# Performance work log

Measured on AMD Instinct MI355X. Metric: run time of the kernel, lower is better.

Reference implementation:

```python
import jax, jax.numpy as jnp
import numpy as np

L, H, C, HS, E, K, V, BS = 2, 12, 768, 64, 8, 2, 32000, 1024
B, T = 2, 1024


def layer_norm(x, s, b):
    mu = x.mean(-1, keepdims=True)
    var = ((x - mu) ** 2).mean(-1, keepdims=True)
    return (x - mu) / jnp.sqrt(var + 1e-5) * s + b


def setup_inputs() -> dict:
    key = jax.random.key(0)
    ks = jax.random.split(key, 16)
    def n(k, shape, s=0.02):
        return jax.random.normal(k, shape, dtype=jnp.float32) * s
    return {
        'idx': jax.random.randint(ks[0], (B, T), 0, V),
        'targets': jax.random.randint(ks[1], (B, T), 0, V),
        'tok_emb': n(ks[2], (V, C)),
        'pos_emb': n(ks[3], (BS, C)),
        'ln1_s': jnp.ones((L, C), jnp.float32), 'ln1_b': jnp.zeros((L, C), jnp.float32),
        'wq': n(ks[4], (L, H, C, HS)), 'wk': n(ks[5], (L, H, C, HS)), 'wv': n(ks[6], (L, H, C, HS)),
        'wo': n(ks[7], (L, C, C)), 'bo': jnp.zeros((L, C), jnp.float32),
        'ln2_s': jnp.ones((L, C), jnp.float32), 'ln2_b': jnp.zeros((L, C), jnp.float32),
        'gate_w': n(ks[8], (L, E, C)),
        'w1': n(ks[9], (L, E, 4 * C, C)), 'b1': jnp.zeros((L, E, 4 * C), jnp.float32),
        'w2': n(ks[10], (L, E, C, 4 * C)), 'b2': jnp.zeros((L, E, C), jnp.float32),
        'lm_w': n(ks[11], (V, C)), 'lm_b': jnp.zeros((V,), jnp.float32),
    }


def reference(idx, targets, tok_emb, pos_emb, ln1_s, ln1_b, wq, wk, wv, wo, bo,
              ln2_s, ln2_b, gate_w, w1, b1, w2, b2, lm_w, lm_b):
    Bsz, Tn = idx.shape
    x = tok_emb[idx] + pos_emb[:Tn]                       # [B,T,C]
    mask = jnp.tril(jnp.ones((Tn, Tn), bool))
    for l in range(L):
        # causal multi-head attention (per-head projections, scale = n_embed**-0.5 as in source)
        h = layer_norm(x, ln1_s[l], ln1_b[l])
        q = jnp.einsum('btc,hcd->bhtd', h, wq[l])
        k = jnp.einsum('btc,hcd->bhtd', h, wk[l])
        v = jnp.einsum('btc,hcd->bhtd', h, wv[l])
        att = jnp.einsum('bhtd,bhsd->bhts', q, k) * (C ** -0.5)
        att = jax.nn.softmax(jnp.where(mask, att, -jnp.inf), axis=-1)
        o = jnp.einsum('bhts,bhsd->bhtd', att, v)
        o = o.transpose(0, 2, 1, 3).reshape(Bsz, Tn, C)   # concat heads
        x = x + jnp.einsum('btc,oc->bto', o, wo[l]) + bo[l]
        # MoE FFN: top-k routing, softmax over selected gate logits
        h2 = layer_norm(x, ln2_s[l], ln2_b[l]).reshape(-1, C)     # [N,C]
        gl = jnp.einsum('tc,ec->te', h2, gate_w[l])               # [N,E]
        wts, sel = jax.lax.top_k(gl, K)
        wts = jax.nn.softmax(wts, axis=-1)
        comb = jnp.einsum('tk,tke->te', wts, jax.nn.one_hot(sel, E, dtype=wts.dtype))
        hid = jax.nn.relu(jnp.einsum('tc,efc->etf', h2, w1[l]) + b1[l][:, None, :])
        y = jnp.einsum('etf,ecf->etc', hid, w2[l]) + b2[l][:, None, :]
        moe = jnp.einsum('te,etc->tc', comb, y)                   # dispatch-weighted combine
        x = x + moe.reshape(Bsz, Tn, C)
    logits = jnp.einsum('btc,vc->btv', x, lm_w) + lm_b
    lf = logits.reshape(-1, V)
    tf = targets.reshape(-1)
    loss = -jnp.take_along_axis(jax.nn.log_softmax(lf, axis=-1), tf[:, None], axis=1).mean()
    return lf, loss
```

## Files before the change

### kernel.cpp

```cpp
#include <hip/hip_runtime.h>
#include <hip/hip_bf16.h>

#define LCNT 2
#define HCNT 12
#define CDIM 768
#define HSD  64
#define ECNT 8
#define VOC  32000
#define BB   2
#define TT   1024
#define NTOK 2048
#define FF   3072
#define QKVLD 2304
#define TOTCAP 5120

typedef __attribute__((ext_vector_type(8))) short bf16x8;
typedef __attribute__((ext_vector_type(4))) float f32x4;

__device__ __forceinline__ float wave_sum(float v) {
    #pragma unroll
    for (int off = 32; off; off >>= 1) v += __shfl_xor(v, off);
    return v;
}
__device__ __forceinline__ float wave_max(float v) {
    #pragma unroll
    for (int off = 32; off; off >>= 1) v = fmaxf(v, __shfl_xor(v, off));
    return v;
}
__device__ __forceinline__ unsigned short f2bf(float f) {
    unsigned int u = __float_as_uint(f);
    unsigned int r = (u + 0x7FFFu + ((u >> 16) & 1u)) >> 16;
    return (unsigned short)r;
}
__device__ __forceinline__ float bf2f(unsigned short h) {
    return __uint_as_float((unsigned int)h << 16);
}
__device__ __forceinline__ void split2(float a, unsigned short& h, unsigned short& l) {
    h = f2bf(a);
    l = f2bf(a - bf2f(h));
}
__device__ __forceinline__ ushort4 cvt4(float4 v) {
    ushort4 r;
    r.x = f2bf(v.x); r.y = f2bf(v.y); r.z = f2bf(v.z); r.w = f2bf(v.w);
    return r;
}
__device__ __forceinline__ void gload16(const void* g, void* l) {
    __builtin_amdgcn_global_load_lds(
        (const __attribute__((address_space(1))) unsigned int*)g,
        (__attribute__((address_space(3))) unsigned int*)l,
        16, 0, 0);
}

__global__ __launch_bounds__(256)
void cvt_bf16_kernel(const float* __restrict__ in, unsigned short* __restrict__ out, int n4)
{
    for (int i = blockIdx.x * 256 + threadIdx.x; i < n4; i += gridDim.x * 256) {
        float4 v = reinterpret_cast<const float4*>(in)[i];
        reinterpret_cast<ushort4*>(out)[i] = cvt4(v);
    }
}

__global__ __launch_bounds__(256)
void splitw_kernel(const float* __restrict__ in, unsigned short* __restrict__ oh,
                   unsigned short* __restrict__ ol, int n4)
{
    for (int i = blockIdx.x * 256 + threadIdx.x; i < n4; i += gridDim.x * 256) {
        float4 v = reinterpret_cast<const float4*>(in)[i];
        ushort4 h, l;
        split2(v.x, h.x, l.x); split2(v.y, h.y, l.y);
        split2(v.z, h.z, l.z); split2(v.w, h.w, l.w);
        reinterpret_cast<ushort4*>(oh)[i] = h;
        reinterpret_cast<ushort4*>(ol)[i] = l;
    }
}

__global__ __launch_bounds__(256)
void embed_kernel(const int* __restrict__ idx, const float* __restrict__ tok,
                  const float* __restrict__ pos, float* __restrict__ x)
{
    int i = blockIdx.x * 256 + threadIdx.x;
    int c = i % CDIM;
    int n = i / CDIM;
    int t = n % TT;
    x[i] = tok[(size_t)idx[n] * CDIM + c] + pos[(size_t)t * CDIM + c];
}

__global__ __launch_bounds__(256)
void repack_kernel(const float* __restrict__ wq, const float* __restrict__ wk,
                   const float* __restrict__ wv, unsigned short* __restrict__ wph,
                   unsigned short* __restrict__ wpl)
{
    int i = blockIdx.x * 256 + threadIdx.x;
    int kk = i % CDIM;
    int n  = (i / CDIM) % CDIM;
    int w3 = (i / (CDIM * CDIM)) % 3;
    int l  = i / (CDIM * CDIM * 3);
    const float* src = (w3 == 0) ? wq : (w3 == 1) ? wk : wv;
    int h = n / HSD, d = n % HSD;
    float v = src[((((size_t)l * HCNT + h) * CDIM) + kk) * HSD + d];
    unsigned short hh, ll;
    split2(v, hh, ll);
    size_t o = (((size_t)l * 3 + w3) * CDIM + n) * CDIM + kk;
    wph[o] = hh;
    wpl[o] = ll;
}

__global__ __launch_bounds__(256)
void ln_kernel(const float* __restrict__ x, const float* __restrict__ sc,
               const float* __restrict__ bs, float* __restrict__ out)
{
    int row = blockIdx.x;
    const float* xr = x + (size_t)row * CDIM;
    float* orow = out + (size_t)row * CDIM;
    int tid = threadIdx.x;
    float v0 = xr[tid], v1 = xr[tid + 256], v2 = xr[tid + 512];
    float s1 = v0 + v1 + v2;
    float s2 = v0 * v0 + v1 * v1 + v2 * v2;
    s1 = wave_sum(s1);
    s2 = wave_sum(s2);
    __shared__ float r1[4], r2[4];
    int w = tid >> 6, lane = tid & 63;
    if (lane == 0) { r1[w] = s1; r2[w] = s2; }
    __syncthreads();
    float t1 = r1[0] + r1[1] + r1[2] + r1[3];
    float t2 = r2[0] + r2[1] + r2[2] + r2[3];
    float mu = t1 * (1.0f / CDIM);
    float var = t2 * (1.0f / CDIM) - mu * mu;
    float rstd = rsqrtf(var + 1e-5f);
    orow[tid]       = (v0 - mu) * rstd * sc[tid]       + bs[tid];
    orow[tid + 256] = (v1 - mu) * rstd * sc[tid + 256] + bs[tid + 256];
    orow[tid + 512] = (v2 - mu) * rstd * sc[tid + 512] + bs[tid + 512];
}

#define BM 128
#define BN 128
#define BK 32
#define PADK 40

template<int MODE, bool SPLIT>
__global__ __launch_bounds__(256)
void gemm_bf16_kernel(int Kd,
                      const float* __restrict__ A, int lda,
                      const float* __restrict__ B, int ldb,
                      const float* __restrict__ bias,
                      float* __restrict__ out, int ldo,
                      const int* __restrict__ rowmeta,
                      size_t bstride, int biasstride)
{
    __shared__ short Ah[BM * PADK];
    __shared__ short Bh[BN * PADK];
    __shared__ short Al[SPLIT ? BM * PADK : 2];
    __shared__ short Bl[SPLIT ? BN * PADK : 2];

    int roff = 0;
    if (rowmeta) {
        const int ee = blockIdx.z;
        const int rcnt = rowmeta[2 * ee + 1];
        if ((int)(blockIdx.y * BM) >= rcnt) return;
        roff = rowmeta[2 * ee];
        B += (size_t)ee * bstride;
        if (bias) bias += (size_t)ee * biasstride;
    }

    const int tid = threadIdx.x;
    const int m0 = roff + blockIdx.y * BM;
    const int n0 = blockIdx.x * BN;
    const int w = tid >> 6, lane = tid & 63;
    const int wr = w >> 1, wc = w & 1;
    const int lrow = lane & 15, lkg = lane >> 4;
    const int srow = tid >> 3, skg = (tid & 7) * 4;

    const float* Ablk = A + (size_t)m0 * lda;
    const float* Bblk = B + (size_t)n0 * ldb;

    float4 pa[4], pb[4];
    #pragma unroll
    for (int p = 0; p < 4; ++p) {
        pa[p] = *(const float4*)(Ablk + (size_t)(p * 32 + srow) * lda + skg);
        pb[p] = *(const float4*)(Bblk + (size_t)(p * 32 + srow) * ldb + skg);
    }

    f32x4 acc[4][4] = {};
    const int nk = Kd / BK;

    for (int t = 0; t < nk; ++t) {
        __syncthreads();
        #pragma unroll
        for (int p = 0; p < 4; ++p) {
            if constexpr (SPLIT) {
                ushort4 h, l;
                split2(pa[p].x, h.x, l.x); split2(pa[p].y, h.y, l.y);
                split2(pa[p].z, h.z, l.z); split2(pa[p].w, h.w, l.w);
                *(ushort4*)(&Ah[(p * 32 + srow) * PADK + skg]) = h;
                *(ushort4*)(&Al[(p * 32 + srow) * PADK + skg]) = l;
                split2(pb[p].x, h.x, l.x); split2(pb[p].y, h.y, l.y);
                split2(pb[p].z, h.z, l.z); split2(pb[p].w, h.w, l.w);
                *(ushort4*)(&Bh[(p * 32 + srow) * PADK + skg]) = h;
                *(ushort4*)(&Bl[(p * 32 + srow) * PADK + skg]) = l;
            } else {
                *(ushort4*)(&Ah[(p * 32 + srow) * PADK + skg]) = cvt4(pa[p]);
                *(ushort4*)(&Bh[(p * 32 + srow) * PADK + skg]) = cvt4(pb[p]);
            }
        }
        __syncthreads();
        if (t + 1 < nk) {
            const int kb = (t + 1) * BK + skg;
            #pragma unroll
            for (int p = 0; p < 4; ++p) {
                pa[p] = *(const float4*)(Ablk + (size_t)(p * 32 + srow) * lda + kb);
                pb[p] = *(const float4*)(Bblk + (size_t)(p * 32 + srow) * ldb + kb);
            }
        }
        bf16x8 afh[4], afl[4];
        #pragma unroll
        for (int i = 0; i < 4; ++i) {
            afh[i] = *(const bf16x8*)(&Ah[(wr * 64 + i * 16 + lrow) * PADK + lkg * 8]);
            if constexpr (SPLIT)
                afl[i] = *(const bf16x8*)(&Al[(wr * 64 + i * 16 + lrow) * PADK + lkg * 8]);
        }
        #pragma unroll
        for (int j = 0; j < 4; ++j) {
            const bf16x8 bh = *(const bf16x8*)(&Bh[(wc * 64 + j * 16 + lrow) * PADK + lkg * 8]);
            if constexpr (SPLIT) {
                const bf16x8 bl = *(const bf16x8*)(&Bl[(wc * 64 + j * 16 + lrow) * PADK + lkg * 8]);
                #pragma unroll
                for (int i = 0; i < 4; ++i) {
                    acc[i][j] = __builtin_amdgcn_mfma_f32_16x16x32_bf16(afh[i], bh, acc[i][j], 0, 0, 0);
                    acc[i][j] = __builtin_amdgcn_mfma_f32_16x16x32_bf16(afl[i], bh, acc[i][j], 0, 0, 0);
                    acc[i][j] = __builtin_amdgcn_mfma_f32_16x16x32_bf16(afh[i], bl, acc[i][j], 0, 0, 0);
                }
            } else {
                #pragma unroll
                for (int i = 0; i < 4; ++i)
                    acc[i][j] = __builtin_amdgcn_mfma_f32_16x16x32_bf16(afh[i], bh, acc[i][j], 0, 0, 0);
            }
        }
    }

    #pragma unroll
    for (int i = 0; i < 4; ++i) {
        #pragma unroll
        for (int r = 0; r < 4; ++r) {
            const int row = m0 + wr * 64 + i * 16 + lkg * 4 + r;
            #pragma unroll
            for (int j = 0; j < 4; ++j) {
                const int col = n0 + wc * 64 + j * 16 + lrow;
                const float bj = bias ? bias[col] : 0.0f;
                const float vres = acc[i][j][r] + bj;
                float* op = out + (size_t)row * ldo + col;
                if (MODE == 0) *op = vres;
                else if (MODE == 1) *op = *op + vres;
                else *op = fmaxf(vres, 0.0f);
            }
        }
    }
}

template<int MODE>
__global__ __launch_bounds__(256)
void gemm_splitpb_kernel(int Kd,
                         const float* __restrict__ A, int lda,
                         const unsigned short* __restrict__ Bhg,
                         const unsigned short* __restrict__ Blg, int ldb,
                         const float* __restrict__ bias,
                         float* __restrict__ out, int ldo)
{
    __shared__ short Ah[BM * PADK];
    __shared__ short Al[BM * PADK];
    __shared__ short Bh[BN * PADK];
    __shared__ short Bl[BN * PADK];

    const int tid = threadIdx.x;
    const int m0 = blockIdx.y * BM;
    const int n0 = blockIdx.x * BN;
    const int w = tid >> 6, lane = tid & 63;
    const int wr = w >> 1, wc = w & 1;
    const int lrow = lane & 15, lkg = lane >> 4;
    const int srow = tid >> 3, skg = (tid & 7) * 4;

    const float* Ablk = A + (size_t)m0 * lda;
    const unsigned short* Bhblk = Bhg + (size_t)n0 * ldb;
    const unsigned short* Blblk = Blg + (size_t)n0 * ldb;

    float4 pa[4];
    ushort4 pbh[4], pbl[4];
    #pragma unroll
    for (int p = 0; p < 4; ++p) {
        pa[p]  = *(const float4*)(Ablk + (size_t)(p * 32 + srow) * lda + skg);
        pbh[p] = *(const ushort4*)(Bhblk + (size_t)(p * 32 + srow) * ldb + skg);
        pbl[p] = *(const ushort4*)(Blblk + (size_t)(p * 32 + srow) * ldb + skg);
    }

    f32x4 acc[4][4] = {};
    const int nk = Kd / BK;

    for (int t = 0; t < nk; ++t) {
        __syncthreads();
        #pragma unroll
        for (int p = 0; p < 4; ++p) {
            ushort4 h, l;
            split2(pa[p].x, h.x, l.x); split2(pa[p].y, h.y, l.y);
            split2(pa[p].z, h.z, l.z); split2(pa[p].w, h.w, l.w);
            *(ushort4*)(&Ah[(p * 32 + srow) * PADK + skg]) = h;
            *(ushort4*)(&Al[(p * 32 + srow) * PADK + skg]) = l;
            *(ushort4*)(&Bh[(p * 32 + srow) * PADK + skg]) = pbh[p];
            *(ushort4*)(&Bl[(p * 32 + srow) * PADK + skg]) = pbl[p];
        }
        __syncthreads();
        if (t + 1 < nk) {
            const int kb = (t + 1) * BK + skg;
            #pragma unroll
            for (int p = 0; p < 4; ++p) {
                pa[p]  = *(const float4*)(Ablk + (size_t)(p * 32 + srow) * lda + kb);
                pbh[p] = *(const ushort4*)(Bhblk + (size_t)(p * 32 + srow) * ldb + kb);
                pbl[p] = *(const ushort4*)(Blblk + (size_t)(p * 32 + srow) * ldb + kb);
            }
        }
        bf16x8 afh[4], afl[4];
        #pragma unroll
        for (int i = 0; i < 4; ++i) {
            afh[i] = *(const bf16x8*)(&Ah[(wr * 64 + i * 16 + lrow) * PADK + lkg * 8]);
            afl[i] = *(const bf16x8*)(&Al[(wr * 64 + i * 16 + lrow) * PADK + lkg * 8]);
        }
        #pragma unroll
        for (int j = 0; j < 4; ++j) {
            const bf16x8 bh = *(const bf16x8*)(&Bh[(wc * 64 + j * 16 + lrow) * PADK + lkg * 8]);
            const bf16x8 bl = *(const bf16x8*)(&Bl[(wc * 64 + j * 16 + lrow) * PADK + lkg * 8]);
            #pragma unroll
            for (int i = 0; i < 4; ++i) {
                acc[i][j] = __builtin_amdgcn_mfma_f32_16x16x32_bf16(afh[i], bh, acc[i][j], 0, 0, 0);
                acc[i][j] = __builtin_amdgcn_mfma_f32_16x16x32_bf16(afl[i], bh, acc[i][j], 0, 0, 0);
                acc[i][j] = __builtin_amdgcn_mfma_f32_16x16x32_bf16(afh[i], bl, acc[i][j], 0, 0, 0);
            }
        }
    }

    #pragma unroll
    for (int i = 0; i < 4; ++i) {
        #pragma unroll
        for (int r = 0; r < 4; ++r) {
            const int row = m0 + wr * 64 + i * 16 + lkg * 4 + r;
            #pragma unroll
            for (int j = 0; j < 4; ++j) {
                const int col = n0 + wc * 64 + j * 16 + lrow;
                const float bj = bias ? bias[col] : 0.0f;
                const float vres = acc[i][j][r] + bj;
                float* op = out + (size_t)row * ldo + col;
                if (MODE == 0) *op = vres;
                else *op = *op + vres;
            }
        }
    }
}

template<int MODE, bool SWZ, bool OUTBF, bool BBF>
__global__ __launch_bounds__(256)
void gemm_fastw_kernel(int Kd,
                       const unsigned short* __restrict__ A, int lda,
                       const void* __restrict__ Bv, int ldb,
                       const float* __restrict__ bias,
                       void* __restrict__ outv, int ldo,
                       const int* __restrict__ rowmeta,
                       size_t bstride, int biasstride)
{
    __shared__ short Ah[BM * PADK];
    __shared__ short Bh[BN * PADK];

    int bx = blockIdx.x, by = blockIdx.y;
    if constexpr (SWZ) {
        const int nwg = gridDim.x * gridDim.y;
        const int chunk = nwg >> 3;
        const int flat = by * gridDim.x + bx;
        const int newid = (flat & 7) * chunk + (flat >> 3);
        by = newid % gridDim.y;
        bx = newid / gridDim.y;
    }

    const float* Bf = (const float*)Bv;
    const unsigned short* Bb = (const unsigned short*)Bv;
    float* outf = (float*)outv;
    unsigned short* outb = (unsigned short*)outv;

    int roff = 0;
    if (rowmeta) {
        const int ee = blockIdx.z;
        const int rcnt = rowmeta[2 * ee + 1];
        if ((int)(by * BM) >= rcnt) return;
        roff = rowmeta[2 * ee];
        if (BBF) Bb += (size_t)ee * bstride; else Bf += (size_t)ee * bstride;
        if (bias) bias += (size_t)ee * biasstride;
    }

    const int tid = threadIdx.x;
    const int m0 = roff + by * BM;
    const int n0 = bx * BN;
    const int w = tid >> 6, lane = tid & 63;
    const int wr = w >> 1, wc = w & 1;
    const int lrow = lane & 15, lkg = lane >> 4;
    const int srow = tid >> 3, skg = (tid & 7) * 4;

    const unsigned short* Ablk = A + (size_t)m0 * lda;
    const float* Bfblk = Bf + (size_t)n0 * ldb;
    const unsigned short* Bbblk = Bb + (size_t)n0 * ldb;

    ushort4 pa[4];
    ushort4 pbb[4];
    float4  pbf[4];
    #pragma unroll
    for (int p = 0; p < 4; ++p) {
        pa[p] = *(const ushort4*)(Ablk + (size_t)(p * 32 + srow) * lda + skg);
        if constexpr (BBF) pbb[p] = *(const ushort4*)(Bbblk + (size_t)(p * 32 + srow) * ldb + skg);
        else               pbf[p] = *(const float4*)(Bfblk + (size_t)(p * 32 + srow) * ldb + skg);
    }

    f32x4 acc[4][4] = {};
    const int nk = Kd / BK;

    for (int t = 0; t < nk; ++t) {
        __syncthreads();
        #pragma unroll
        for (int p = 0; p < 4; ++p) {
            *(ushort4*)(&Ah[(p * 32 + srow) * PADK + skg]) = pa[p];
            *(ushort4*)(&Bh[(p * 32 + srow) * PADK + skg]) = BBF ? pbb[p] : cvt4(pbf[p]);
        }
        __syncthreads();
        if (t + 1 < nk) {
            const int kb = (t + 1) * BK + skg;
            #pragma unroll
            for (int p = 0; p < 4; ++p) {
                pa[p] = *(const ushort4*)(Ablk + (size_t)(p * 32 + srow) * lda + kb);
                if constexpr (BBF) pbb[p] = *(const ushort4*)(Bbblk + (size_t)(p * 32 + srow) * ldb + kb);
                else               pbf[p] = *(const float4*)(Bfblk + (size_t)(p * 32 + srow) * ldb + kb);
            }
        }
        bf16x8 af[4];
        #pragma unroll
        for (int i = 0; i < 4; ++i)
            af[i] = *(const bf16x8*)(&Ah[(wr * 64 + i * 16 + lrow) * PADK + lkg * 8]);
        #pragma unroll
        for (int j = 0; j < 4; ++j) {
            const bf16x8 bh = *(const bf16x8*)(&Bh[(wc * 64 + j * 16 + lrow) * PADK + lkg * 8]);
            #pragma unroll
            for (int i = 0; i < 4; ++i)
                acc[i][j] = __builtin_amdgcn_mfma_f32_16x16x32_bf16(af[i], bh, acc[i][j], 0, 0, 0);
        }
    }

    #pragma unroll
    for (int i = 0; i < 4; ++i) {
        #pragma unroll
        for (int r = 0; r < 4; ++r) {
            const int row = m0 + wr * 64 + i * 16 + lkg * 4 + r;
            #pragma unroll
            for (int j = 0; j < 4; ++j) {
                const int col = n0 + wc * 64 + j * 16 + lrow;
                const float bj = bias ? bias[col] : 0.0f;
                float vres = acc[i][j][r] + bj;
                if (MODE == 2) vres = fmaxf(vres, 0.0f);
                if constexpr (OUTBF) outb[(size_t)row * ldo + col] = f2bf(vres);
                else                 outf[(size_t)row * ldo + col] = vres;
            }
        }
    }
}

template<bool SWZ>
__global__ __launch_bounds__(256)
void gemm_lds_kernel(int Kd,
                     const unsigned short* __restrict__ A, int lda,
                     const unsigned short* __restrict__ B, int ldb,
                     const float* __restrict__ bias,
                     float* __restrict__ out, int ldo)
{
    __shared__ unsigned short Asl[BM * BK];
    __shared__ unsigned short Bsl[BN * BK];

    int bx = blockIdx.x, by = blockIdx.y;
    if constexpr (SWZ) {
        const int nwg = gridDim.x * gridDim.y;
        const int chunk = nwg >> 3;
        const int flat = by * gridDim.x + bx;
        const int newid = (flat & 7) * chunk + (flat >> 3);
        by = newid % gridDim.y;
        bx = newid / gridDim.y;
    }

    const int tid = threadIdx.x;
    const int m0 = by * BM;
    const int n0 = bx * BN;
    const int w = tid >> 6, lane = tid & 63;
    const int wr = w >> 1, wc = w & 1;
    const int lrow = lane & 15, lkg = lane >> 4;
    const int grow = lane >> 2, gcol = (lane & 3) * 8;

    const unsigned short* Ablk = A + (size_t)m0 * lda;
    const unsigned short* Bblk = B + (size_t)n0 * ldb;

    f32x4 acc[4][4] = {};
    const int nk = Kd / BK;

    for (int t = 0; t < nk; ++t) {
        const int k0 = t * BK;
        __syncthreads();
        #pragma unroll
        for (int j = 0; j < 2; ++j) {
            const int rbase = w * 32 + j * 16;
            gload16(Ablk + (size_t)(rbase + grow) * lda + k0 + gcol, Asl + rbase * BK);
            gload16(Bblk + (size_t)(rbase + grow) * ldb + k0 + gcol, Bsl + rbase * BK);
        }
        __syncthreads();

        bf16x8 af[4];
        #pragma unroll
        for (int i = 0; i < 4; ++i)
            af[i] = *(const bf16x8*)(Asl + (wr * 64 + i * 16 + lrow) * BK + lkg * 8);
        #pragma unroll
        for (int j = 0; j < 4; ++j) {
            const bf16x8 bh = *(const bf16x8*)(Bsl + (wc * 64 + j * 16 + lrow) * BK + lkg * 8);
            #pragma unroll
            for (int i = 0; i < 4; ++i)
                acc[i][j] = __builtin_amdgcn_mfma_f32_16x16x32_bf16(af[i], bh, acc[i][j], 0, 0, 0);
        }
    }

    #pragma unroll
    for (int i = 0; i < 4; ++i) {
        #pragma unroll
        for (int r = 0; r < 4; ++r) {
            const int row = m0 + wr * 64 + i * 16 + lkg * 4 + r;
            #pragma unroll
            for (int j = 0; j < 4; ++j) {
                const int col = n0 + wc * 64 + j * 16 + lrow;
                const float bj = bias ? bias[col] : 0.0f;
                out[(size_t)row * ldo + col] = acc[i][j][r] + bj;
            }
        }
    }
}

#define QBLK 64
#define KVBLK 64

__global__ __launch_bounds__(256)
void attn_mfma_kernel(const float* __restrict__ qkv, float* __restrict__ o)
{
    __shared__ short Kh[2][KVBLK][PADK];
    __shared__ short Kl[2][KVBLK][PADK];
    __shared__ short Vh[2][HSD][PADK];
    __shared__ short Vl[2][HSD][PADK];
    __shared__ short Ph[4][2][16][PADK];
    __shared__ short Pl[4][2][16][PADK];

    const int t0 = blockIdx.x * QBLK;
    const int bh = blockIdx.y;
    const int b = bh / HCNT, hh = bh % HCNT;
    const size_t baseq = (size_t)b * TT * QKVLD + (size_t)hh * HSD;
    const size_t obase = (size_t)b * TT * CDIM + (size_t)hh * HSD;
    const float* q = qkv + baseq;
    const float* k = qkv + baseq + CDIM;
    const float* v = qkv + baseq + 2 * CDIM;
    const int tid = threadIdx.x;
    const int w = tid >> 6, lane = tid & 63;
    const int lrow = lane & 15, lkg = lane >> 4;
    const float sscale = rsqrtf((float)CDIM);

    bf16x8 qh[2], ql[2];
    {
        const float* qr = q + (size_t)(t0 + w * 16 + lrow) * QKVLD;
        #pragma unroll
        for (int ks = 0; ks < 2; ++ks) {
            #pragma unroll
            for (int j = 0; j < 8; ++j) {
                unsigned short h, l;
                split2(qr[ks * 32 + lkg * 8 + j], h, l);
                qh[ks][j] = (short)h;
                ql[ks][j] = (short)l;
            }
        }
    }

    f32x4 oacc[4] = {};
    float m_[4], l_[4];
    #pragma unroll
    for (int rr = 0; rr < 4; ++rr) { m_[rr] = -1e30f; l_[rr] = 0.0f; }

    for (int s0 = 0; s0 <= t0 + QBLK - 1; s0 += KVBLK) {
        __syncthreads();
        {
            const int srow = tid >> 3, skg = (tid & 7) * 4;
            #pragma unroll
            for (int p = 0; p < 2; ++p) {
                const float* krow = k + (size_t)(s0 + p * 32 + srow) * QKVLD;
                #pragma unroll
                for (int ks = 0; ks < 2; ++ks) {
                    float4 a = *(const float4*)(krow + ks * 32 + skg);
                    ushort4 h, l;
                    split2(a.x, h.x, l.x); split2(a.y, h.y, l.y);
                    split2(a.z, h.z, l.z); split2(a.w, h.w, l.w);
                    *(ushort4*)(&Kh[ks][p * 32 + srow][skg]) = h;
                    *(ushort4*)(&Kl[ks][p * 32 + srow][skg]) = l;
                }
            }
            const int key = tid & 63, dg = (tid >> 6) * 16;
            const float* vrow = v + (size_t)(s0 + key) * QKVLD + dg;
            const int kst = key >> 5, ko = key & 31;
            #pragma unroll
            for (int dd = 0; dd < 16; dd += 4) {
                float4 a = *(const float4*)(vrow + dd);
                unsigned short h, l;
                split2(a.x, h, l); Vh[kst][dg + dd + 0][ko] = h; Vl[kst][dg + dd + 0][ko] = l;
                split2(a.y, h, l); Vh[kst][dg + dd + 1][ko] = h; Vl[kst][dg + dd + 1][ko] = l;
                split2(a.z, h, l); Vh[kst][dg + dd + 2][ko] = h; Vl[kst][dg + dd + 2][ko] = l;
                split2(a.w, h, l); Vh[kst][dg + dd + 3][ko] = h; Vl[kst][dg + dd + 3][ko] = l;
            }
        }
        __syncthreads();

        f32x4 sacc[4] = {};
        #pragma unroll
        for (int j = 0; j < 4; ++j) {
            #pragma unroll
            for (int ks = 0; ks < 2; ++ks) {
                const bf16x8 bh = *(const bf16x8*)(&Kh[ks][j * 16 + lrow][lkg * 8]);
                const bf16x8 bl = *(const bf16x8*)(&Kl[ks][j * 16 + lrow][lkg * 8]);
                sacc[j] = __builtin_amdgcn_mfma_f32_16x16x32_bf16(qh[ks], bh, sacc[j], 0, 0, 0);
                sacc[j] = __builtin_amdgcn_mfma_f32_16x16x32_bf16(ql[ks], bh, sacc[j], 0, 0, 0);
                sacc[j] = __builtin_amdgcn_mfma_f32_16x16x32_bf16(qh[ks], bl, sacc[j], 0, 0, 0);
            }
        }

        #pragma unroll
        for (int rr = 0; rr < 4; ++rr) {
            const int qi = t0 + w * 16 + lkg * 4 + rr;
            float pv[4];
            float mx = -1e30f;
            #pragma unroll
            for (int j = 0; j < 4; ++j) {
                float s = sacc[j][rr] * sscale;
                if (s0 + j * 16 + lrow > qi) s = -1e30f;
                pv[j] = s;
                mx = fmaxf(mx, s);
            }
            #pragma unroll
            for (int off = 1; off < 16; off <<= 1) mx = fmaxf(mx, __shfl_xor(mx, off));
            const float mnew = fmaxf(m_[rr], mx);
            const float corr = __expf(m_[rr] - mnew);
            float ps = 0.0f;
            #pragma unroll
            for (int j = 0; j < 4; ++j) { pv[j] = __expf(pv[j] - mnew); ps += pv[j]; }
            #pragma unroll
            for (int off = 1; off < 16; off <<= 1) ps += __shfl_xor(ps, off);
            l_[rr] = l_[rr] * corr + ps;
            m_[rr] = mnew;
            #pragma unroll
            for (int jd = 0; jd < 4; ++jd) oacc[jd][rr] *= corr;
            #pragma unroll
            for (int j = 0; j < 4; ++j) {
                unsigned short h, l;
                split2(pv[j], h, l);
                const int key = j * 16 + lrow;
                Ph[w][key >> 5][lkg * 4 + rr][key & 31] = h;
                Pl[w][key >> 5][lkg * 4 + rr][key & 31] = l;
            }
        }

        #pragma unroll
        for (int ks = 0; ks < 2; ++ks) {
            const bf16x8 ah = *(const bf16x8*)(&Ph[w][ks][lrow][lkg * 8]);
            const bf16x8 al = *(const bf16x8*)(&Pl[w][ks][lrow][lkg * 8]);
            #pragma unroll
            for (int jd = 0; jd < 4; ++jd) {
                const bf16x8 bh = *(const bf16x8*)(&Vh[ks][jd * 16 + lrow][lkg * 8]);
                const bf16x8 bl = *(const bf16x8*)(&Vl[ks][jd * 16 + lrow][lkg * 8]);
                oacc[jd] = __builtin_amdgcn_mfma_f32_16x16x32_bf16(ah, bh, oacc[jd], 0, 0, 0);
                oacc[jd] = __builtin_amdgcn_mfma_f32_16x16x32_bf16(al, bh, oacc[jd], 0, 0, 0);
                oacc[jd] = __builtin_amdgcn_mfma_f32_16x16x32_bf16(ah, bl, oacc[jd], 0, 0, 0);
            }
        }
    }

    #pragma unroll
    for (int rr = 0; rr < 4; ++rr) {
        const int qi = t0 + w * 16 + lkg * 4 + rr;
        const float invl = 1.0f / l_[rr];
        float* orow = o + obase + (size_t)qi * CDIM;
        #pragma unroll
        for (int jd = 0; jd < 4; ++jd)
            orow[jd * 16 + lrow] = oacc[jd][rr] * invl;
    }
}

__global__ __launch_bounds__(256)
void gate_kernel(const float* __restrict__ h2, const float* __restrict__ gw,
                 int2* __restrict__ sel, float2* __restrict__ wts)
{
    __shared__ float gws[ECNT * CDIM];
    int tid = threadIdx.x;
    for (int i = tid; i < ECNT * CDIM; i += 256) gws[i] = gw[i];
    __syncthreads();
    int t = blockIdx.x * 256 + tid;
    const float* hr = h2 + (size_t)t * CDIM;
    float g[ECNT] = {};
    for (int c = 0; c < CDIM; ++c) {
        float hv = hr[c];
        #pragma unroll
        for (int e = 0; e < ECNT; ++e) g[e] = fmaf(hv, gws[e * CDIM + c], g[e]);
    }
    int e0 = 0; float g0 = g[0];
    #pragma unroll
    for (int e = 1; e < ECNT; ++e) if (g[e] > g0) { g0 = g[e]; e0 = e; }
    int e1 = -1; float g1 = -1e30f;
    #pragma unroll
    for (int e = 0; e < ECNT; ++e) if (e != e0 && g[e] > g1) { g1 = g[e]; e1 = e; }
    float z = __expf(g1 - g0);
    float w0 = 1.0f / (1.0f + z);
    sel[t] = make_int2(e0, e1);
    wts[t] = make_float2(w0, 1.0f - w0);
}

__global__ __launch_bounds__(256)
void route_kernel(const int2* __restrict__ sel, int* __restrict__ perm,
                  int* __restrict__ tokpos, int* __restrict__ meta)
{
    __shared__ int cnt[ECNT], off[ECNT], cur[ECNT];
    const int tid = threadIdx.x;
    if (tid < ECNT) cnt[tid] = 0;
    __syncthreads();
    for (int t = tid; t < NTOK; t += 256) {
        atomicAdd(&cnt[sel[t].x], 1);
        atomicAdd(&cnt[sel[t].y], 1);
    }
    __syncthreads();
    if (tid == 0) {
        int run = 0;
        for (int e = 0; e < ECNT; ++e) {
            off[e] = run; cur[e] = 0;
            int pc = (cnt[e] + BM - 1) / BM * BM;
            meta[2 * e] = run; meta[2 * e + 1] = pc;
            run += pc;
        }
    }
    __syncthreads();
    for (int p = tid; p < TOTCAP; p += 256) perm[p] = 0;
    __syncthreads();
    for (int t = tid; t < NTOK; t += 256) {
        int2 s = sel[t];
        int p0 = atomicAdd(&cur[s.x], 1); perm[off[s.x] + p0] = t; tokpos[2 * t]     = off[s.x] + p0;
        int p1 = atomicAdd(&cur[s.y], 1); perm[off[s.y] + p1] = t; tokpos[2 * t + 1] = off[s.y] + p1;
    }
}

__global__ __launch_bounds__(256)
void gather_kernel(const float* __restrict__ h2, const int* __restrict__ perm,
                   float* __restrict__ xg)
{
    int i = blockIdx.x * 256 + threadIdx.x;
    int c = i % CDIM, p = i / CDIM;
    xg[i] = h2[(size_t)perm[p] * CDIM + c];
}

__global__ __launch_bounds__(256)
void gather_bf16_kernel(const float* __restrict__ h2, const int* __restrict__ perm,
                        unsigned short* __restrict__ xg)
{
    int i = blockIdx.x * 256 + threadIdx.x;
    int c = i % CDIM, p = i / CDIM;
    xg[i] = f2bf(h2[(size_t)perm[p] * CDIM + c]);
}

__global__ __launch_bounds__(256)
void combine_kernel(const float* __restrict__ y, const int* __restrict__ tokpos,
                    const float2* __restrict__ wts, float* __restrict__ x)
{
    int i = blockIdx.x * 256 + threadIdx.x;
    int c = i % CDIM, t = i / CDIM;
    float2 wv = wts[t];
    x[i] += wv.x * y[(size_t)tokpos[2 * t] * CDIM + c]
          + wv.y * y[(size_t)tokpos[2 * t + 1] * CDIM + c];
}

__global__ __launch_bounds__(256)
void loss_row_kernel(const float* __restrict__ logits, const int* __restrict__ tgt,
                     float* __restrict__ lrow)
{
    int row = blockIdx.x;
    const float* lr = logits + (size_t)row * VOC;
    int tid = threadIdx.x, w = tid >> 6, lane = tid & 63;
    __shared__ float red[4];
    float mx = -1e30f;
    for (int i = tid; i < VOC; i += 256) mx = fmaxf(mx, lr[i]);
    mx = wave_max(mx);
    if (lane == 0) red[w] = mx;
    __syncthreads();
    mx = fmaxf(fmaxf(red[0], red[1]), fmaxf(red[2], red[3]));
    __syncthreads();
    float se = 0.0f;
    for (int i = tid; i < VOC; i += 256) se += expf(lr[i] - mx);
    se = wave_sum(se);
    if (lane == 0) red[w] = se;
    __syncthreads();
    if (tid == 0) {
        float lse = mx + logf(red[0] + red[1] + red[2] + red[3]);
        lrow[row] = lse - lr[tgt[row]];
    }
}

__global__ __launch_bounds__(256)
void loss_reduce_kernel(const float* __restrict__ lrow, float* __restrict__ out)
{
    int tid = threadIdx.x, w = tid >> 6, lane = tid & 63;
    float s = 0.0f;
    for (int i = tid; i < NTOK; i += 256) s += lrow[i];
    s = wave_sum(s);
    __shared__ float red[4];
    if (lane == 0) red[w] = s;
    __syncthreads();
    if (tid == 0) out[0] = (red[0] + red[1] + red[2] + red[3]) * (1.0f / NTOK);
}

extern "C" void kernel_launch(void* const* d_in, const int* in_sizes, int n_in,
                              void* d_out, int out_size, void* d_ws, size_t ws_size,
                              hipStream_t stream)
{
    const int*   idx     = (const int*)d_in[0];
    const int*   targets = (const int*)d_in[1];
    const float* tok_emb = (const float*)d_in[2];
    const float* pos_emb = (const float*)d_in[3];
    const float* ln1_s   = (const float*)d_in[4];
    const float* ln1_b   = (const float*)d_in[5];
    const float* wq      = (const float*)d_in[6];
    const float* wk      = (const float*)d_in[7];
    const float* wv      = (const float*)d_in[8];
    const float* wo      = (const float*)d_in[9];
    const float* bo      = (const float*)d_in[10];
    const float* ln2_s   = (const float*)d_in[11];
    const float* ln2_b   = (const float*)d_in[12];
    const float* gate_w  = (const float*)d_in[13];
    const float* w1      = (const float*)d_in[14];
    const float* b1      = (const float*)d_in[15];
    const float* w2      = (const float*)d_in[16];
    const float* b2      = (const float*)d_in[17];
    const float* lm_w    = (const float*)d_in[18];
    const float* lm_b    = (const float*)d_in[19];
    float* out = (float*)d_out;

    unsigned short* wph = (unsigned short*)d_ws;
    unsigned short* wpl = wph + (size_t)3 * LCNT * CDIM * CDIM;
    unsigned short* woh = wpl + (size_t)3 * LCNT * CDIM * CDIM;
    unsigned short* wol = woh + (size_t)LCNT * CDIM * CDIM;
    float* x    = (float*)(wol + (size_t)LCNT * CDIM * CDIM);
    float* hbuf = x    + (size_t)NTOK * CDIM;
    float* qkv  = hbuf + (size_t)NTOK * CDIM;
    float* xg   = qkv  + (size_t)NTOK * QKVLD;
    float* hid  = xg   + (size_t)TOTCAP * CDIM;
    float* lrow = hid  + (size_t)TOTCAP * FF;
    float2* wts = (float2*)(lrow + NTOK);
    int2*  sel  = (int2*)(wts + NTOK);
    int*   perm = (int*)(sel + NTOK);
    int*  tokpos= perm + TOTCAP;
    int*   meta = tokpos + 2 * NTOK;
    unsigned short* x_bf = (unsigned short*)(meta + 16);

    unsigned short* xg_bf  = (unsigned short*)xg;
    unsigned short* hid_bf = (unsigned short*)hid;
    unsigned short* lmw_bf = (unsigned short*)hid;

    dim3 blk(256);

    repack_kernel<<<(3 * LCNT * CDIM * CDIM) / 256, blk, 0, stream>>>(wq, wk, wv, wph, wpl);
    splitw_kernel<<<1024, blk, 0, stream>>>(wo, woh, wol, LCNT * CDIM * CDIM / 4);
    embed_kernel<<<(NTOK * CDIM) / 256, blk, 0, stream>>>(idx, tok_emb, pos_emb, x);

    for (int l = 0; l < LCNT; ++l) {
        ln_kernel<<<NTOK, blk, 0, stream>>>(x, ln1_s + (size_t)l * CDIM, ln1_b + (size_t)l * CDIM, hbuf);

        gemm_splitpb_kernel<0><<<dim3(QKVLD / BN, NTOK / BM), blk, 0, stream>>>(
            CDIM, hbuf, CDIM, wph + (size_t)l * 3 * CDIM * CDIM, wpl + (size_t)l * 3 * CDIM * CDIM,
            CDIM, nullptr, qkv, QKVLD);

        attn_mfma_kernel<<<dim3(TT / QBLK, BB * HCNT), blk, 0, stream>>>(qkv, hbuf);

        gemm_splitpb_kernel<1><<<dim3(CDIM / BN, NTOK / BM), blk, 0, stream>>>(
            CDIM, hbuf, CDIM, woh + (size_t)l * CDIM * CDIM, wol + (size_t)l * CDIM * CDIM,
            CDIM, bo + (size_t)l * CDIM, x, CDIM);

        float* h2 = qkv;
        float* ybuf = qkv;
        ln_kernel<<<NTOK, blk, 0, stream>>>(x, ln2_s + (size_t)l * CDIM, ln2_b + (size_t)l * CDIM, h2);
        gate_kernel<<<NTOK / 256, blk, 0, stream>>>(h2, gate_w + (size_t)l * ECNT * CDIM, sel, wts);
        route_kernel<<<1, blk, 0, stream>>>(sel, perm, tokpos, meta);

        const float* w1l = w1 + (size_t)l * ECNT * FF * CDIM;
        const float* b1l = b1 + (size_t)l * ECNT * FF;
        const float* w2l = w2 + (size_t)l * ECNT * CDIM * FF;
        const float* b2l = b2 + (size_t)l * ECNT * CDIM;
        if (l == 0) {
            gather_kernel<<<(TOTCAP * CDIM) / 256, blk, 0, stream>>>(h2, perm, xg);
            gemm_bf16_kernel<2, true><<<dim3(FF / BN, TOTCAP / BM, ECNT), blk, 0, stream>>>(
                CDIM, xg, CDIM, w1l, CDIM, b1l, hid, FF, meta, (size_t)FF * CDIM, FF);
            gemm_bf16_kernel<0, true><<<dim3(CDIM / BN, TOTCAP / BM, ECNT), blk, 0, stream>>>(
                FF, hid, FF, w2l, FF, b2l, ybuf, CDIM, meta, (size_t)CDIM * FF, CDIM);
        } else {
            gather_bf16_kernel<<<(TOTCAP * CDIM) / 256, blk, 0, stream>>>(h2, perm, xg_bf);
            gemm_fastw_kernel<2, false, true, false><<<dim3(FF / BN, TOTCAP / BM, ECNT), blk, 0, stream>>>(
                CDIM, xg_bf, CDIM, w1l, CDIM, b1l, hid_bf, FF, meta, (size_t)FF * CDIM, FF);
            gemm_fastw_kernel<0, false, false, false><<<dim3(CDIM / BN, TOTCAP / BM, ECNT), blk, 0, stream>>>(
                FF, hid_bf, FF, w2l, FF, b2l, ybuf, CDIM, meta, (size_t)CDIM * FF, CDIM);
        }
        combine_kernel<<<(NTOK * CDIM) / 256, blk, 0, stream>>>(ybuf, tokpos, wts, x);
    }

    cvt_bf16_kernel<<<2048, blk, 0, stream>>>(lm_w, lmw_bf, VOC * CDIM / 4);
    cvt_bf16_kernel<<<512, blk, 0, stream>>>(x, x_bf, NTOK * CDIM / 4);

    gemm_lds_kernel<true><<<dim3(VOC / BN, NTOK / BM), blk, 0, stream>>>(
        CDIM, x_bf, CDIM, lmw_bf, CDIM, lm_b, out, VOC);

    loss_row_kernel<<<NTOK, blk, 0, stream>>>(out, targets, lrow);
    loss_reduce_kernel<<<1, blk, 0, stream>>>(lrow, out + (size_t)NTOK * VOC);
}
```

Measured before the change: 1.409 ms.

## Split-K the layer-0 expert down-projection and pre-split QKV to bf16 hi/lo

```diff
diff --git a/kernel.cpp b/kernel.cpp
--- a/kernel.cpp
+++ b/kernel.cpp
@@ -13,6 +13,7 @@
 #define FF   3072
 #define QKVLD 2304
 #define TOTCAP 5120
+#define SKN  4
 
 typedef __attribute__((ext_vector_type(8))) short bf16x8;
 typedef __attribute__((ext_vector_type(4))) float f32x4;
@@ -256,14 +257,118 @@
     }
 }
 
-template<int MODE>
+__global__ __launch_bounds__(256)
+void gemm_sk_kernel(int Kc,
+                    const float* __restrict__ A, int lda,
+                    const float* __restrict__ B, int ldb,
+                    const float* __restrict__ bias,
+                    float* __restrict__ part, int ldo, size_t pstride,
+                    const int* __restrict__ rowmeta,
+                    size_t bstride, int biasstride)
+{
+    __shared__ short Ah[BM * PADK];
+    __shared__ short Bh[BN * PADK];
+    __shared__ short Al[BM * PADK];
+    __shared__ short Bl[BN * PADK];
+
+    const int zz = blockIdx.z;
+    const int ee = zz / SKN, kz = zz % SKN;
+    const int rcnt = rowmeta[2 * ee + 1];
+    if ((int)(blockIdx.y * BM) >= rcnt) return;
+    const int roff = rowmeta[2 * ee];
+    const float* Bp = B + (size_t)ee * bstride + (size_t)kz * Kc;
+    const float* Ap = A + (size_t)kz * Kc;
+    const float* biasp = (kz == 0 && bias) ? bias + (size_t)ee * biasstride : nullptr;
+    float* out = part + (size_t)kz * pstride;
+
+    const int tid = threadIdx.x;
+    const int m0 = roff + blockIdx.y * BM;
+    const int n0 = blockIdx.x * BN;
+    const int w = tid >> 6, lane = tid & 63;
+    const int wr = w >> 1, wc = w & 1;
+    const int lrow = lane & 15, lkg = lane >> 4;
+    const int srow = tid >> 3, skg = (tid & 7) * 4;
+
+    const float* Ablk = Ap + (size_t)m0 * lda;
+    const float* Bblk = Bp + (size_t)n0 * ldb;
+
+    float4 pa[4], pb[4];
+    #pragma unroll
+    for (int p = 0; p < 4; ++p) {
+        pa[p] = *(const float4*)(Ablk + (size_t)(p * 32 + srow) * lda + skg);
+        pb[p] = *(const float4*)(Bblk + (size_t)(p * 32 + srow) * ldb + skg);
+    }
+
+    f32x4 acc[4][4] = {};
+    const int nk = Kc / BK;
+
+    for (int t = 0; t < nk; ++t) {
+        __syncthreads();
+        #pragma unroll
+        for (int p = 0; p < 4; ++p) {
+            ushort4 h, l;
+            split2(pa[p].x, h.x, l.x); split2(pa[p].y, h.y, l.y);
+            split2(pa[p].z, h.z, l.z); split2(pa[p].w, h.w, l.w);
+            *(ushort4*)(&Ah[(p * 32 + srow) * PADK + skg]) = h;
+            *(ushort4*)(&Al[(p * 32 + srow) * PADK + skg]) = l;
+            split2(pb[p].x, h.x, l.x); split2(pb[p].y, h.y, l.y);
+            split2(pb[p].z, h.z, l.z); split2(pb[p].w, h.w, l.w);
+            *(ushort4*)(&Bh[(p * 32 + srow) * PADK + skg]) = h;
+            *(ushort4*)(&Bl[(p * 32 + srow) * PADK + skg]) = l;
+        }
+        __syncthreads();
+        if (t + 1 < nk) {
+            const int kb = (t + 1) * BK + skg;
+            #pragma unroll
+            for (int p = 0; p < 4; ++p) {
+                pa[p] = *(const float4*)(Ablk + (size_t)(p * 32 + srow) * lda + kb);
+                pb[p] = *(const float4*)(Bblk + (size_t)(p * 32 + srow) * ldb + kb);
+            }
+        }
+        bf16x8 afh[4], afl[4];
+        #pragma unroll
+        for (int i = 0; i < 4; ++i) {
+            afh[i] = *(const bf16x8*)(&Ah[(wr * 64 + i * 16 + lrow) * PADK + lkg * 8]);
+            afl[i] = *(const bf16x8*)(&Al[(wr * 64 + i * 16 + lrow) * PADK + lkg * 8]);
+        }
+        #pragma unroll
+        for (int j = 0; j < 4; ++j) {
+            const bf16x8 bh = *(const bf16x8*)(&Bh[(wc * 64 + j * 16 + lrow) * PADK + lkg * 8]);
+            const bf16x8 bl = *(const bf16x8*)(&Bl[(wc * 64 + j * 16 + lrow) * PADK + lkg * 8]);
+            #pragma unroll
+            for (int i = 0; i < 4; ++i) {
+                acc[i][j] = __builtin_amdgcn_mfma_f32_16x16x32_bf16(afh[i], bh, acc[i][j], 0, 0, 0);
+                acc[i][j] = __builtin_amdgcn_mfma_f32_16x16x32_bf16(afl[i], bh, acc[i][j], 0, 0, 0);
+                acc[i][j] = __builtin_amdgcn_mfma_f32_16x16x32_bf16(afh[i], bl, acc[i][j], 0, 0, 0);
+            }
+        }
+    }
+
+    #pragma unroll
+    for (int i = 0; i < 4; ++i) {
+        #pragma unroll
+        for (int r = 0; r < 4; ++r) {
+            const int row = m0 + wr * 64 + i * 16 + lkg * 4 + r;
+            #pragma unroll
+            for (int j = 0; j < 4; ++j) {
+                const int col = n0 + wc * 64 + j * 16 + lrow;
+                const float bj = biasp ? biasp[col] : 0.0f;
+                out[(size_t)row * ldo + col] = acc[i][j][r] + bj;
+            }
+        }
+    }
+}
+
+template<int MODE, bool OUTSPLIT>
 __global__ __launch_bounds__(256)
 void gemm_splitpb_kernel(int Kd,
                          const float* __restrict__ A, int lda,
                          const unsigned short* __restrict__ Bhg,
                          const unsigned short* __restrict__ Blg, int ldb,
                          const float* __restrict__ bias,
-                         float* __restrict__ out, int ldo)
+                         float* __restrict__ out,
+                         unsigned short* __restrict__ outh,
+                         unsigned short* __restrict__ outl, int ldo)
 {
     __shared__ short Ah[BM * PADK];
     __shared__ short Al[BM * PADK];
@@ -345,9 +450,16 @@
                 const int col = n0 + wc * 64 + j * 16 + lrow;
                 const float bj = bias ? bias[col] : 0.0f;
                 const float vres = acc[i][j][r] + bj;
-                float* op = out + (size_t)row * ldo + col;
-                if (MODE == 0) *op = vres;
-                else *op = *op + vres;
+                if constexpr (OUTSPLIT) {
+                    unsigned short h, l;
+                    split2(vres, h, l);
+                    outh[(size_t)row * ldo + col] = h;
+                    outl[(size_t)row * ldo + col] = l;
+                } else {
+                    float* op = out + (size_t)row * ldo + col;
+                    if (MODE == 0) *op = vres;
+                    else *op = *op + vres;
+                }
             }
         }
     }
@@ -542,7 +654,9 @@
 #define KVBLK 64
 
 __global__ __launch_bounds__(256)
-void attn_mfma_kernel(const float* __restrict__ qkv, float* __restrict__ o)
+void attn_mfma_kernel(const unsigned short* __restrict__ qh_g,
+                      const unsigned short* __restrict__ ql_g,
+                      float* __restrict__ o)
 {
     __shared__ short Kh[2][KVBLK][PADK];
     __shared__ short Kl[2][KVBLK][PADK];
@@ -556,9 +670,10 @@
     const int b = bh / HCNT, hh = bh % HCNT;
     const size_t baseq = (size_t)b * TT * QKVLD + (size_t)hh * HSD;
     const size_t obase = (size_t)b * TT * CDIM + (size_t)hh * HSD;
-    const float* q = qkv + baseq;
-    const float* k = qkv + baseq + CDIM;
-    const float* v = qkv + baseq + 2 * CDIM;
+    const unsigned short* kh_g = qh_g + baseq + CDIM;
+    const unsigned short* kl_g = ql_g + baseq + CDIM;
+    const unsigned short* vh_g = qh_g + baseq + 2 * CDIM;
+    const unsigned short* vl_g = ql_g + baseq + 2 * CDIM;
     const int tid = threadIdx.x;
     const int w = tid >> 6, lane = tid & 63;
     const int lrow = lane & 15, lkg = lane >> 4;
@@ -566,16 +681,11 @@
 
     bf16x8 qh[2], ql[2];
     {
-        const float* qr = q + (size_t)(t0 + w * 16 + lrow) * QKVLD;
+        const size_t qroff = baseq + (size_t)(t0 + w * 16 + lrow) * QKVLD;
         #pragma unroll
         for (int ks = 0; ks < 2; ++ks) {
-            #pragma unroll
-            for (int j = 0; j < 8; ++j) {
-                unsigned short h, l;
-                split2(qr[ks * 32 + lkg * 8 + j], h, l);
-                qh[ks][j] = (short)h;
-                ql[ks][j] = (short)l;
-            }
+            qh[ks] = *(const bf16x8*)(qh_g + qroff + ks * 32 + lkg * 8);
+            ql[ks] = *(const bf16x8*)(ql_g + qroff + ks * 32 + lkg * 8);
         }
     }
 
@@ -590,28 +700,24 @@
             const int srow = tid >> 3, skg = (tid & 7) * 4;
             #pragma unroll
             for (int p = 0; p < 2; ++p) {
-                const float* krow = k + (size_t)(s0 + p * 32 + srow) * QKVLD;
+                const size_t kroff = (size_t)(s0 + p * 32 + srow) * QKVLD;
                 #pragma unroll
                 for (int ks = 0; ks < 2; ++ks) {
-                    float4 a = *(const float4*)(krow + ks * 32 + skg);
-                    ushort4 h, l;
-                    split2(a.x, h.x, l.x); split2(a.y, h.y, l.y);
-                    split2(a.z, h.z, l.z); split2(a.w, h.w, l.w);
-                    *(ushort4*)(&Kh[ks][p * 32 + srow][skg]) = h;
-                    *(ushort4*)(&Kl[ks][p * 32 + srow][skg]) = l;
+                    *(ushort4*)(&Kh[ks][p * 32 + srow][skg]) = *(const ushort4*)(kh_g + kroff + ks * 32 + skg);
+                    *(ushort4*)(&Kl[ks][p * 32 + srow][skg]) = *(const ushort4*)(kl_g + kroff + ks * 32 + skg);
                 }
             }
             const int key = tid & 63, dg = (tid >> 6) * 16;
-            const float* vrow = v + (size_t)(s0 + key) * QKVLD + dg;
+            const size_t vroff = (size_t)(s0 + key) * QKVLD + dg;
             const int kst = key >> 5, ko = key & 31;
             #pragma unroll
             for (int dd = 0; dd < 16; dd += 4) {
-                float4 a = *(const float4*)(vrow + dd);
-                unsigned short h, l;
-                split2(a.x, h, l); Vh[kst][dg + dd + 0][ko] = h; Vl[kst][dg + dd + 0][ko] = l;
-                split2(a.y, h, l); Vh[kst][dg + dd + 1][ko] = h; Vl[kst][dg + dd + 1][ko] = l;
-                split2(a.z, h, l); Vh[kst][dg + dd + 2][ko] = h; Vl[kst][dg + dd + 2][ko] = l;
-                split2(a.w, h, l); Vh[kst][dg + dd + 3][ko] = h; Vl[kst][dg + dd + 3][ko] = l;
+                ushort4 hv = *(const ushort4*)(vh_g + vroff + dd);
+                ushort4 lv = *(const ushort4*)(vl_g + vroff + dd);
+                Vh[kst][dg + dd + 0][ko] = hv.x; Vl[kst][dg + dd + 0][ko] = lv.x;
+                Vh[kst][dg + dd + 1][ko] = hv.y; Vl[kst][dg + dd + 1][ko] = lv.y;
+                Vh[kst][dg + dd + 2][ko] = hv.z; Vl[kst][dg + dd + 2][ko] = lv.z;
+                Vh[kst][dg + dd + 3][ko] = hv.w; Vl[kst][dg + dd + 3][ko] = lv.w;
             }
         }
         __syncthreads();
@@ -768,15 +874,24 @@
     xg[i] = f2bf(h2[(size_t)perm[p] * CDIM + c]);
 }
 
-__global__ __launch_bounds__(256)
-void combine_kernel(const float* __restrict__ y, const int* __restrict__ tokpos,
+template<int SK>
+__global__ __launch_bounds__(256)
+void combine_kernel(const float* __restrict__ y, size_t pstride,
+                    const int* __restrict__ tokpos,
                     const float2* __restrict__ wts, float* __restrict__ x)
 {
     int i = blockIdx.x * 256 + threadIdx.x;
     int c = i % CDIM, t = i / CDIM;
     float2 wv = wts[t];
-    x[i] += wv.x * y[(size_t)tokpos[2 * t] * CDIM + c]
-          + wv.y * y[(size_t)tokpos[2 * t + 1] * CDIM + c];
+    const size_t r0 = (size_t)tokpos[2 * t] * CDIM + c;
+    const size_t r1 = (size_t)tokpos[2 * t + 1] * CDIM + c;
+    float a0 = 0.0f, a1 = 0.0f;
+    #pragma unroll
+    for (int s = 0; s < SK; ++s) {
+        a0 += y[s * pstride + r0];
+        a1 += y[s * pstride + r1];
+    }
+    x[i] += wv.x * a0 + wv.y * a1;
 }
 
 __global__ __launch_bounds__(256)
@@ -860,7 +975,13 @@
     int*  tokpos= perm + TOTCAP;
     int*   meta = tokpos + 2 * NTOK;
     unsigned short* x_bf = (unsigned short*)(meta + 16);
-
+    float* part = (float*)(x_bf + (size_t)NTOK * CDIM);
+
+    const size_t need_bytes = (size_t)((char*)(part + (size_t)SKN * TOTCAP * CDIM) - (char*)d_ws);
+    const bool use_sk = ws_size >= need_bytes;
+
+    unsigned short* qkvh = (unsigned short*)qkv;
+    unsigned short* qkvl = qkvh + (size_t)NTOK * QKVLD;
     unsigned short* xg_bf  = (unsigned short*)xg;
     unsigned short* hid_bf = (unsigned short*)hid;
     unsigned short* lmw_bf = (unsigned short*)hid;
@@ -874,15 +995,15 @@
     for (int l = 0; l < LCNT; ++l) {
         ln_kernel<<<NTOK, blk, 0, stream>>>(x, ln1_s + (size_t)l * CDIM, ln1_b + (size_t)l * CDIM, hbuf);
 
-        gemm_splitpb_kernel<0><<<dim3(QKVLD / BN, NTOK / BM), blk, 0, stream>>>(
+        gemm_splitpb_kernel<0, true><<<dim3(QKVLD / BN, NTOK / BM), blk, 0, stream>>>(
             CDIM, hbuf, CDIM, wph + (size_t)l * 3 * CDIM * CDIM, wpl + (size_t)l * 3 * CDIM * CDIM,
-            CDIM, nullptr, qkv, QKVLD);
-
-        attn_mfma_kernel<<<dim3(TT / QBLK, BB * HCNT), blk, 0, stream>>>(qkv, hbuf);
-
-        gemm_splitpb_kernel<1><<<dim3(CDIM / BN, NTOK / BM), blk, 0, stream>>>(
+            CDIM, nullptr, nullptr, qkvh, qkvl, QKVLD);
+
+        attn_mfma_kernel<<<dim3(TT / QBLK, BB * HCNT), blk, 0, stream>>>(qkvh, qkvl, hbuf);
+
+        gemm_splitpb_kernel<1, false><<<dim3(CDIM / BN, NTOK / BM), blk, 0, stream>>>(
             CDIM, hbuf, CDIM, woh + (size_t)l * CDIM * CDIM, wol + (size_t)l * CDIM * CDIM,
-            CDIM, bo + (size_t)l * CDIM, x, CDIM);
+            CDIM, bo + (size_t)l * CDIM, x, nullptr, nullptr, CDIM);
 
         float* h2 = qkv;
         float* ybuf = qkv;
@@ -898,16 +1019,27 @@
             gather_kernel<<<(TOTCAP * CDIM) / 256, blk, 0, stream>>>(h2, perm, xg);
             gemm_bf16_kernel<2, true><<<dim3(FF / BN, TOTCAP / BM, ECNT), blk, 0, stream>>>(
                 CDIM, xg, CDIM, w1l, CDIM, b1l, hid, FF, meta, (size_t)FF * CDIM, FF);
-            gemm_bf16_kernel<0, true><<<dim3(CDIM / BN, TOTCAP / BM, ECNT), blk, 0, stream>>>(
-                FF, hid, FF, w2l, FF, b2l, ybuf, CDIM, meta, (size_t)CDIM * FF, CDIM);
+            if (use_sk) {
+                gemm_sk_kernel<<<dim3(CDIM / BN, TOTCAP / BM, ECNT * SKN), blk, 0, stream>>>(
+                    FF / SKN, hid, FF, w2l, FF, b2l, part, CDIM, (size_t)TOTCAP * CDIM,
+                    meta, (size_t)CDIM * FF, CDIM);
+                combine_kernel<SKN><<<(NTOK * CDIM) / 256, blk, 0, stream>>>(
+                    part, (size_t)TOTCAP * CDIM, tokpos, wts, x);
+            } else {
+                gemm_bf16_kernel<0, true><<<dim3(CDIM / BN, TOTCAP / BM, ECNT), blk, 0, stream>>>(
+                    FF, hid, FF, w2l, FF, b2l, ybuf, CDIM, meta, (size_t)CDIM * FF, CDIM);
+                combine_kernel<1><<<(NTOK * CDIM) / 256, blk, 0, stream>>>(
+                    ybuf, 0, tokpos, wts, x);
+            }
         } else {
             gather_bf16_kernel<<<(TOTCAP * CDIM) / 256, blk, 0, stream>>>(h2, perm, xg_bf);
             gemm_fastw_kernel<2, false, true, false><<<dim3(FF / BN, TOTCAP / BM, ECNT), blk, 0, stream>>>(
                 CDIM, xg_bf, CDIM, w1l, CDIM, b1l, hid_bf, FF, meta, (size_t)FF * CDIM, FF);
             gemm_fastw_kernel<0, false, false, false><<<dim3(CDIM / BN, TOTCAP / BM, ECNT), blk, 0, stream>>>(
                 FF, hid_bf, FF, w2l, FF, b2l, ybuf, CDIM, meta, (size_t)CDIM * FF, CDIM);
-        }
-        combine_kernel<<<(NTOK * CDIM) / 256, blk, 0, stream>>>(ybuf, tokpos, wts, x);
+            combine_kernel<1><<<(NTOK * CDIM) / 256, blk, 0, stream>>>(
+                ybuf, 0, tokpos, wts, x);
+        }
     }
 
     cvt_bf16_kernel<<<2048, blk, 0, stream>>>(lm_w, lmw_bf, VOC * CDIM / 4);
```

After: 1.372 ms. -2.6%, faster.
